# Kernel optimization log

Measured on AMD Instinct MI355X. Metric: run time of the kernel, lower is better.

The kernel has to match this reference:

```python
import jax, jax.numpy as jnp
import numpy as np

L, H, C, T_BLOCK, V = 12, 12, 768, 1024, 50257
EPS = 1e-5


def setup_inputs() -> dict:
    key = jax.random.key(0)
    ks = jax.random.split(key, 16)
    s = 0.02
    inp = {
        "idx": jax.random.randint(ks[0], (4, 1024), 0, V),
        "wte": jax.random.normal(ks[1], (V, C), jnp.float32) * s,
        "wpe": jax.random.normal(ks[2], (T_BLOCK, C), jnp.float32) * s,
        "ln1_w": jnp.ones((L, C), jnp.float32),
        "ln1_b": jnp.zeros((L, C), jnp.float32),
        "w_qkv": jax.random.normal(ks[3], (L, C, 3 * C), jnp.float32) * s,
        "b_qkv": jnp.zeros((L, 3 * C), jnp.float32),
        "w_ao": jax.random.normal(ks[4], (L, C, C), jnp.float32) * s,
        "b_ao": jnp.zeros((L, C), jnp.float32),
        "ln2_w": jnp.ones((L, C), jnp.float32),
        "ln2_b": jnp.zeros((L, C), jnp.float32),
        "w_fc": jax.random.normal(ks[5], (L, C, 4 * C), jnp.float32) * s,
        "b_fc": jnp.zeros((L, 4 * C), jnp.float32),
        "w_fp": jax.random.normal(ks[6], (L, 4 * C, C), jnp.float32) * s,
        "b_fp": jnp.zeros((L, C), jnp.float32),
        "lnf_w": jnp.ones((C,), jnp.float32),
        "lnf_b": jnp.zeros((C,), jnp.float32),
        "w_head": jax.random.normal(ks[7], (C, 1), jnp.float32) * s,
    }
    return inp


def _ln(x, w, b):
    mu = jnp.mean(x, axis=-1, keepdims=True)
    var = jnp.var(x, axis=-1, keepdims=True)
    return (x - mu) * jax.lax.rsqrt(var + EPS) * w + b


def _gpt_forward(idx, wte, wpe, ln1_w, ln1_b, w_qkv, b_qkv, w_ao, b_ao,
                 ln2_w, ln2_b, w_fc, b_fc, w_fp, b_fp, lnf_w, lnf_b, w_head):
    B, T = idx.shape
    D = C // H  # head dim
    x = wte[idx] + wpe[:T]  # [B,T,C]
    causal = jnp.tril(jnp.ones((T, T), bool))  # [T,T]

    def block(x, p):
        l1w, l1b, wq, bq, wo, bo, l2w, l2b, wf, bf, wp, bp = p
        h = _ln(x, l1w, l1b)
        qkv = h @ wq + bq  # [B,T,3C]
        q, k, v = jnp.split(qkv, 3, axis=-1)
        q = q.reshape(B, T, H, D).transpose(0, 2, 1, 3)  # [B,H,T,D]
        k = k.reshape(B, T, H, D).transpose(0, 2, 1, 3)
        v = v.reshape(B, T, H, D).transpose(0, 2, 1, 3)
        att = jnp.einsum('bhqd,bhkd->bhqk', q, k) * (1.0 / np.sqrt(D))
        att = jnp.where(causal, att, -jnp.inf)
        att = jax.nn.softmax(att, axis=-1)
        y = jnp.einsum('bhqk,bhkd->bhqd', att, v)
        y = y.transpose(0, 2, 1, 3).reshape(B, T, C)
        x = x + (y @ wo + bo)
        h2 = _ln(x, l2w, l2b)
        x = x + (jax.nn.gelu(h2 @ wf + bf, approximate=True) @ wp + bp)
        return x, None

    layer_params = (ln1_w, ln1_b, w_qkv, b_qkv, w_ao, b_ao,
                    ln2_w, ln2_b, w_fc, b_fc, w_fp, b_fp)
    x, _ = jax.lax.scan(block, x, layer_params)
    x = _ln(x, lnf_w, lnf_b)
    return x @ w_head  # [B,T,1]


def reference(idx, wte, wpe, ln1_w, ln1_b, w_qkv, b_qkv, w_ao, b_ao,
              ln2_w, ln2_b, w_fc, b_fc, w_fp, b_fp, lnf_w, lnf_b, w_head):
    return _gpt_forward(idx, wte, wpe, ln1_w, ln1_b, w_qkv, b_qkv, w_ao, b_ao,
                        ln2_w, ln2_b, w_fc, b_fc, w_fp, b_fp, lnf_w, lnf_b, w_head)
```

## Files before the change

kernel.cpp:

```cpp
#include <hip/hip_runtime.h>


#define CN    768
#define NKV   2304
#define FCN   3072
#define TN    1024
#define BN    4
#define HN    12
#define NL    12
#define MTOT  4096

typedef __attribute__((ext_vector_type(4))) float f32x4;
typedef __attribute__((ext_vector_type(8))) short short8;
typedef __attribute__((ext_vector_type(4))) unsigned short u16x4;

typedef const __attribute__((address_space(1))) void* gas_t;
typedef __attribute__((address_space(3))) void* las_t;

__device__ __forceinline__ unsigned short f2b(float f) {
    unsigned int u = __float_as_uint(f);
    u += 0x7fffu + ((u >> 16) & 1u);
    return (unsigned short)(u >> 16);
}
__device__ __forceinline__ float b2f(unsigned short h) {
    return __uint_as_float(((unsigned int)h) << 16);
}

__device__ __forceinline__ void gemm128(
        const unsigned short* __restrict__ A, int lda,
        const unsigned short* __restrict__ B, int ldb,
        int m0, int n0, int kbeg, int kend, f32x4 acc[4][4])
{
    __shared__ __align__(16) unsigned short As[128 * 32];
    __shared__ __align__(16) unsigned short Bs[128 * 32];
    const int tid  = threadIdx.x;
    const int wave = tid >> 6;
    const int lane = tid & 63;
    const int quad = lane >> 4;
    const int l16  = lane & 15;
    const int wm   = (wave & 1) * 64;
    const int wn   = (wave >> 1) * 64;
    const int srow = wave * 16 + (lane >> 2);
    const int scol = (lane & 3) << 3;
    const unsigned short* ag = A + (long)(m0 + srow) * lda + scol;
    const unsigned short* bg = B + (long)(n0 + srow) * ldb + scol;
    unsigned short* asw = As + wave * 512;
    unsigned short* bsw = Bs + wave * 512;

    for (int k0 = kbeg; k0 < kend; k0 += 32) {
        __syncthreads();
        __builtin_amdgcn_global_load_lds((gas_t)(ag + k0),                  (las_t)(asw),            16, 0, 0);
        __builtin_amdgcn_global_load_lds((gas_t)(ag + k0 + (long)64 * lda), (las_t)(asw + 64 * 32),  16, 0, 0);
        __builtin_amdgcn_global_load_lds((gas_t)(bg + k0),                  (las_t)(bsw),            16, 0, 0);
        __builtin_amdgcn_global_load_lds((gas_t)(bg + k0 + (long)64 * ldb), (las_t)(bsw + 64 * 32),  16, 0, 0);
        __syncthreads();
        short8 af[4], bf[4];
#pragma unroll
        for (int i = 0; i < 4; ++i)
            af[i] = *(const short8*)(As + (wm + i * 16 + l16) * 32 + quad * 8);
#pragma unroll
        for (int j = 0; j < 4; ++j)
            bf[j] = *(const short8*)(Bs + (wn + j * 16 + l16) * 32 + quad * 8);
#pragma unroll
        for (int i = 0; i < 4; ++i)
#pragma unroll
            for (int j = 0; j < 4; ++j)
                acc[i][j] = __builtin_amdgcn_mfma_f32_16x16x32_bf16(af[i], bf[j], acc[i][j], 0, 0, 0);
    }
}

__global__ __launch_bounds__(256) void k_qkv128(
        const unsigned short* __restrict__ A, const unsigned short* __restrict__ B,
        const float* __restrict__ bias,
        unsigned short* __restrict__ qb, unsigned short* __restrict__ kb,
        unsigned short* __restrict__ vt)
{
    f32x4 acc[4][4];
#pragma unroll
    for (int i = 0; i < 4; ++i)
#pragma unroll
        for (int j = 0; j < 4; ++j) acc[i][j] = 0.f;
    const int m0 = blockIdx.x * 128, n0 = blockIdx.y * 128;
    gemm128(A, CN, B, CN, m0, n0, 0, CN, acc);
    const int wave = threadIdx.x >> 6, lane = threadIdx.x & 63;
    const int quad = lane >> 4, l16 = lane & 15;
    const int wm = (wave & 1) * 64, wn = (wave >> 1) * 64;
#pragma unroll
    for (int j = 0; j < 4; ++j) {
        int col = n0 + wn + j * 16 + l16;
        float bv = bias[col];
        int which = col / CN;
        int cc = col - which * CN;
        int h = cc >> 6, d = cc & 63;
#pragma unroll
        for (int i = 0; i < 4; ++i) {
#pragma unroll
            for (int r = 0; r < 4; ++r) {
                int row = m0 + wm + i * 16 + quad * 4 + r;
                int b = row >> 10, t = row & 1023;
                int bh = b * HN + h;
                unsigned short val = f2b(acc[i][j][r] + bv);
                if (which == 0)      qb[(bh * TN + t) * 64 + d] = val;
                else if (which == 1) kb[(bh * TN + t) * 64 + d] = val;
                else                 vt[(bh * 64 + d) * TN + t] = val;
            }
        }
    }
}

__global__ __launch_bounds__(256) void k_fc128(
        const unsigned short* __restrict__ A, const unsigned short* __restrict__ B,
        const float* __restrict__ bias, unsigned short* __restrict__ G)
{
    f32x4 acc[4][4];
#pragma unroll
    for (int i = 0; i < 4; ++i)
#pragma unroll
        for (int j = 0; j < 4; ++j) acc[i][j] = 0.f;
    const int m0 = blockIdx.x * 128, n0 = blockIdx.y * 128;
    gemm128(A, CN, B, CN, m0, n0, 0, CN, acc);
    const int wave = threadIdx.x >> 6, lane = threadIdx.x & 63;
    const int quad = lane >> 4, l16 = lane & 15;
    const int wm = (wave & 1) * 64, wn = (wave >> 1) * 64;
#pragma unroll
    for (int j = 0; j < 4; ++j) {
        int col = n0 + wn + j * 16 + l16;
        float bv = bias[col];
#pragma unroll
        for (int i = 0; i < 4; ++i)
#pragma unroll
            for (int r = 0; r < 4; ++r) {
                int row = m0 + wm + i * 16 + quad * 4 + r;
                float u = acc[i][j][r] + bv;
                float c = 0.7978845608028654f * (u + 0.044715f * u * u * u);
                float g = 0.5f * u * (1.0f + tanhf(c));
                G[(long)row * FCN + col] = f2b(g);
            }
    }
}

__global__ __launch_bounds__(256) void k_res128(
        const unsigned short* __restrict__ A, int lda,
        const unsigned short* __restrict__ B, int K, int ksplit,
        const float* __restrict__ bias, float* __restrict__ X)
{
    f32x4 acc[4][4];
#pragma unroll
    for (int i = 0; i < 4; ++i)
#pragma unroll
        for (int j = 0; j < 4; ++j) acc[i][j] = 0.f;
    const int m0 = blockIdx.x * 128, n0 = blockIdx.y * 128;
    const int kz = blockIdx.z;
    const int klen = K / ksplit;
    gemm128(A, lda, B, K, m0, n0, kz * klen, kz * klen + klen, acc);
    const int wave = threadIdx.x >> 6, lane = threadIdx.x & 63;
    const int quad = lane >> 4, l16 = lane & 15;
    const int wm = (wave & 1) * 64, wn = (wave >> 1) * 64;
#pragma unroll
    for (int j = 0; j < 4; ++j) {
        int col = n0 + wn + j * 16 + l16;
        float bv = (kz == 0) ? bias[col] : 0.f;
#pragma unroll
        for (int i = 0; i < 4; ++i)
#pragma unroll
            for (int r = 0; r < 4; ++r) {
                int row = m0 + wm + i * 16 + quad * 4 + r;
                atomicAdd(&X[(long)row * CN + col], acc[i][j][r] + bv);
            }
    }
}

__device__ __forceinline__ void flash_qblock(
        int bm,
        const unsigned short* __restrict__ qg, const unsigned short* __restrict__ kg,
        const unsigned short* __restrict__ vg, unsigned short* __restrict__ yb,
        unsigned short* Qs, unsigned short* Ks, unsigned short* Vs,
        unsigned short* Ps)
{
    const int tid  = threadIdx.x;
    const int wave = tid >> 6;
    const int lane = tid & 63;
    const int quad = lane >> 4;
    const int l16  = lane & 15;
    const int r8 = lane >> 3;
    const int sl = lane & 7;

    __syncthreads();

#pragma unroll
    for (int c = 0; c < 4; ++c) {
        int chunk = wave * 4 + c;
        int row = chunk * 8 + r8;
        int slot = sl ^ (row & 7);
        __builtin_amdgcn_global_load_lds(
            (gas_t)(qg + (long)(bm * 128 + row) * 64 + slot * 8),
            (las_t)(Qs + chunk * 512), 16, 0, 0);
    }
    __syncthreads();

    short8 qf[2][2];
#pragma unroll
    for (int i = 0; i < 2; ++i)
#pragma unroll
        for (int ks = 0; ks < 2; ++ks) {
            int row = wave * 32 + i * 16 + l16;
            int slot = (ks * 4 + quad) ^ (row & 7);
            qf[i][ks] = *(const short8*)(Qs + row * 64 + slot * 8);
        }

    f32x4 acc[2][4];
#pragma unroll
    for (int i = 0; i < 2; ++i)
#pragma unroll
        for (int j = 0; j < 4; ++j) acc[i][j] = 0.f;
    float m_run[2][4], l_run[2][4];
#pragma unroll
    for (int i = 0; i < 2; ++i)
#pragma unroll
        for (int r = 0; r < 4; ++r) { m_run[i][r] = -3e38f; l_run[i][r] = 0.f; }

    const int qbase = bm * 128 + wave * 32;
    const int nt = 2 * bm + 2;
    unsigned short* pw = Ps + wave * (32 * 70);

    for (int t = 0; t < nt; ++t) {
        const int k0 = t * 64;
        __syncthreads();
#pragma unroll
        for (int c = 0; c < 2; ++c) {
            int chunk = wave * 2 + c;
            int row = chunk * 8 + r8;
            int slot = sl ^ (row & 7);
            __builtin_amdgcn_global_load_lds(
                (gas_t)(kg + (long)(k0 + row) * 64 + slot * 8),
                (las_t)(Ks + chunk * 512), 16, 0, 0);
            __builtin_amdgcn_global_load_lds(
                (gas_t)(vg + (long)row * TN + k0 + slot * 8),
                (las_t)(Vs + chunk * 512), 16, 0, 0);
        }
        __syncthreads();

        f32x4 s[2][4];
#pragma unroll
        for (int i = 0; i < 2; ++i)
#pragma unroll
            for (int j = 0; j < 4; ++j) s[i][j] = 0.f;
#pragma unroll
        for (int j = 0; j < 4; ++j) {
            int row = j * 16 + l16;
#pragma unroll
            for (int ks = 0; ks < 2; ++ks) {
                int slot = (ks * 4 + quad) ^ (row & 7);
                short8 kf = *(const short8*)(Ks + row * 64 + slot * 8);
#pragma unroll
                for (int i = 0; i < 2; ++i)
                    s[i][j] = __builtin_amdgcn_mfma_f32_16x16x32_bf16(qf[i][ks], kf, s[i][j], 0, 0, 0);
            }
        }

#pragma unroll
        for (int i = 0; i < 2; ++i) {
#pragma unroll
            for (int r = 0; r < 4; ++r) {
                const int qrow = qbase + i * 16 + quad * 4 + r;
                float mx = -3e38f;
#pragma unroll
                for (int j = 0; j < 4; ++j) {
                    float v = s[i][j][r] * 0.125f;
                    if (k0 + j * 16 + l16 > qrow) v = -3e38f;
                    s[i][j][r] = v;
                    mx = fmaxf(mx, v);
                }
#pragma unroll
                for (int o = 1; o < 16; o <<= 1) mx = fmaxf(mx, __shfl_xor(mx, o));
                const float mnew = fmaxf(m_run[i][r], mx);
                const float resc = __expf(m_run[i][r] - mnew);
                m_run[i][r] = mnew;
                float ls = 0.f;
#pragma unroll
                for (int j = 0; j < 4; ++j) {
                    float p = __expf(s[i][j][r] - mnew);
                    s[i][j][r] = p;
                    ls += p;
                }
#pragma unroll
                for (int o = 1; o < 16; o <<= 1) ls += __shfl_xor(ls, o);
                l_run[i][r] = l_run[i][r] * resc + ls;
#pragma unroll
                for (int j = 0; j < 4; ++j)
                    acc[i][j][r] *= resc;
            }
        }

#pragma unroll
        for (int i = 0; i < 2; ++i)
#pragma unroll
            for (int j = 0; j < 4; ++j)
#pragma unroll
                for (int r = 0; r < 4; ++r)
                    pw[(i * 16 + quad * 4 + r) * 70 + j * 16 + l16] = f2b(s[i][j][r]);
        __syncthreads();

        short8 pa[2][2];
#pragma unroll
        for (int i = 0; i < 2; ++i)
#pragma unroll
            for (int ks = 0; ks < 2; ++ks)
                pa[i][ks] = *(const short8*)(pw + (i * 16 + l16) * 70 + ks * 32 + quad * 8);

#pragma unroll
        for (int j = 0; j < 4; ++j) {
            int row = j * 16 + l16;
#pragma unroll
            for (int ks = 0; ks < 2; ++ks) {
                int slot = (ks * 4 + quad) ^ (row & 7);
                short8 vf = *(const short8*)(Vs + row * 64 + slot * 8);
#pragma unroll
                for (int i = 0; i < 2; ++i)
                    acc[i][j] = __builtin_amdgcn_mfma_f32_16x16x32_bf16(pa[i][ks], vf, acc[i][j], 0, 0, 0);
            }
        }
    }

#pragma unroll
    for (int i = 0; i < 2; ++i)
#pragma unroll
        for (int r = 0; r < 4; ++r) {
            const float inv = 1.0f / l_run[i][r];
            const int row = qbase + i * 16 + quad * 4 + r;
#pragma unroll
            for (int j = 0; j < 4; ++j)
                yb[(long)row * CN + j * 16 + l16] = f2b(acc[i][j][r] * inv);
        }
}

__global__ __launch_bounds__(256) void k_attn(
        const unsigned short* __restrict__ qb, const unsigned short* __restrict__ kb,
        const unsigned short* __restrict__ vt, unsigned short* __restrict__ y)
{
    __shared__ __align__(16) unsigned short Qs[128 * 64];
    __shared__ __align__(16) unsigned short Ks[64 * 64];
    __shared__ __align__(16) unsigned short Vs[64 * 64];
    __shared__ __align__(16) unsigned short Ps[4 * 32 * 70];

    const int x = blockIdx.x;
    const int z = blockIdx.z;
    const unsigned short* qg = qb + (long)z * TN * 64;
    const unsigned short* kg = kb + (long)z * TN * 64;
    const unsigned short* vg = vt + (long)z * 64 * TN;
    const int b = z / HN, h = z - b * HN;
    unsigned short* yb = y + (long)b * TN * CN + h * 64;

    flash_qblock(x,     qg, kg, vg, yb, Qs, Ks, Vs, Ps);
    flash_qblock(7 - x, qg, kg, vg, yb, Qs, Ks, Vs, Ps);
}

__global__ __launch_bounds__(256) void k_ln(
        const float* __restrict__ X, const float* __restrict__ w,
        const float* __restrict__ b, unsigned short* __restrict__ O)
{
    const int row  = blockIdx.x * 4 + (threadIdx.x >> 6);
    const int lane = threadIdx.x & 63;
    const f32x4* xr = (const f32x4*)(X + (long)row * CN);
    const f32x4* wv = (const f32x4*)w;
    const f32x4* bv = (const f32x4*)b;
    f32x4 v[3];
    float s = 0.f, sq = 0.f;
#pragma unroll
    for (int i = 0; i < 3; ++i) {
        v[i] = xr[i * 64 + lane];
#pragma unroll
        for (int c = 0; c < 4; ++c) { s += v[i][c]; sq += v[i][c] * v[i][c]; }
    }
#pragma unroll
    for (int o = 32; o > 0; o >>= 1) { s += __shfl_xor(s, o); sq += __shfl_xor(sq, o); }
    const float mu = s * (1.0f / CN);
    const float rstd = rsqrtf(sq * (1.0f / CN) - mu * mu + 1e-5f);
    u16x4* orow = (u16x4*)(O + (long)row * CN);
#pragma unroll
    for (int i = 0; i < 3; ++i) {
        f32x4 wc = wv[i * 64 + lane], bc = bv[i * 64 + lane];
        u16x4 o4;
#pragma unroll
        for (int c = 0; c < 4; ++c) o4[c] = f2b((v[i][c] - mu) * rstd * wc[c] + bc[c]);
        orow[i * 64 + lane] = o4;
    }
}

__global__ __launch_bounds__(256) void k_final(
        const float* __restrict__ X, const float* __restrict__ w,
        const float* __restrict__ b, const float* __restrict__ wh,
        float* __restrict__ out)
{
    const int row  = blockIdx.x * 4 + (threadIdx.x >> 6);
    const int lane = threadIdx.x & 63;
    const f32x4* xr = (const f32x4*)(X + (long)row * CN);
    const f32x4* wv = (const f32x4*)w;
    const f32x4* bv = (const f32x4*)b;
    const f32x4* hv = (const f32x4*)wh;
    f32x4 v[3];
    float s = 0.f, sq = 0.f;
#pragma unroll
    for (int i = 0; i < 3; ++i) {
        v[i] = xr[i * 64 + lane];
#pragma unroll
        for (int c = 0; c < 4; ++c) { s += v[i][c]; sq += v[i][c] * v[i][c]; }
    }
#pragma unroll
    for (int o = 32; o > 0; o >>= 1) { s += __shfl_xor(s, o); sq += __shfl_xor(sq, o); }
    const float mu = s * (1.0f / CN);
    const float rstd = rsqrtf(sq * (1.0f / CN) - mu * mu + 1e-5f);
    float acc = 0.f;
#pragma unroll
    for (int i = 0; i < 3; ++i) {
        f32x4 wc = wv[i * 64 + lane], bc = bv[i * 64 + lane], hc = hv[i * 64 + lane];
#pragma unroll
        for (int c = 0; c < 4; ++c)
            acc += ((v[i][c] - mu) * rstd * wc[c] + bc[c]) * hc[c];
    }
#pragma unroll
    for (int o = 32; o > 0; o >>= 1) acc += __shfl_xor(acc, o);
    if (lane == 0) out[row] = acc;
}

__global__ __launch_bounds__(256) void k_embed(
        const int* __restrict__ idx, const float* __restrict__ wte,
        const float* __restrict__ wpe, float* __restrict__ X)
{
    long i4 = (long)blockIdx.x * 256 + threadIdx.x;
    int c4 = (int)(i4 % (CN / 4));
    int bt = (int)(i4 / (CN / 4));
    int t = bt & 1023;
    int tok = idx[bt];
    f32x4 a = *(const f32x4*)(wte + (long)tok * CN + c4 * 4);
    f32x4 p = *(const f32x4*)(wpe + (long)t * CN + c4 * 4);
    *(f32x4*)(X + (long)bt * CN + c4 * 4) = a + p;
}

__global__ __launch_bounds__(256) void k_transpose(
        const float* __restrict__ in, unsigned short* __restrict__ out, int K, int N)
{
    __shared__ float tile[32][33];
    const int z = blockIdx.z;
    in  += (long)z * K * N;
    out += (long)z * K * N;
    const int n0 = blockIdx.x * 32, k0 = blockIdx.y * 32;
    const int tx = threadIdx.x & 31, ty = threadIdx.x >> 5;
#pragma unroll
    for (int i = 0; i < 4; ++i)
        tile[ty + i * 8][tx] = in[(long)(k0 + ty + i * 8) * N + n0 + tx];
    __syncthreads();
#pragma unroll
    for (int i = 0; i < 4; ++i)
        out[(long)(n0 + ty + i * 8) * K + k0 + tx] = f2b(tile[tx][ty + i * 8]);
}

extern "C" void kernel_launch(void* const* d_in, const int* in_sizes, int n_in,
                              void* d_out, int out_size, void* d_ws, size_t ws_size,
                              hipStream_t stream)
{
    const int*   idx    = (const int*)  d_in[0];
    const float* wte    = (const float*)d_in[1];
    const float* wpe    = (const float*)d_in[2];
    const float* ln1_w  = (const float*)d_in[3];
    const float* ln1_b  = (const float*)d_in[4];
    const float* w_qkv  = (const float*)d_in[5];
    const float* b_qkv  = (const float*)d_in[6];
    const float* w_ao   = (const float*)d_in[7];
    const float* b_ao   = (const float*)d_in[8];
    const float* ln2_w  = (const float*)d_in[9];
    const float* ln2_b  = (const float*)d_in[10];
    const float* w_fc   = (const float*)d_in[11];
    const float* b_fc   = (const float*)d_in[12];
    const float* w_fp   = (const float*)d_in[13];
    const float* b_fp   = (const float*)d_in[14];
    const float* lnf_w  = (const float*)d_in[15];
    const float* lnf_b  = (const float*)d_in[16];
    const float* w_head = (const float*)d_in[17];
    float* out = (float*)d_out;

    char* ws = (char*)d_ws;
    unsigned short* wqkvT = (unsigned short*)(ws + 0L);
    unsigned short* waoT  = (unsigned short*)(ws + 42467328L);
    unsigned short* wfcT  = (unsigned short*)(ws + 56623104L);
    unsigned short* wfpT  = (unsigned short*)(ws + 113246208L);
    float*          x     = (float*)         (ws + 169869312L);
    unsigned short* hb    = (unsigned short*)(ws + 182452224L);
    unsigned short* qb    = (unsigned short*)(ws + 188743680L);
    unsigned short* kb    = (unsigned short*)(ws + 195035136L);
    unsigned short* vt    = (unsigned short*)(ws + 201326592L);
    unsigned short* y     = (unsigned short*)(ws + 308281344L);
    unsigned short* g     = (unsigned short*)(ws + 314572800L);

    hipLaunchKernelGGL(k_transpose, dim3(NKV / 32, CN / 32, NL), dim3(256), 0, stream,
                       w_qkv, wqkvT, CN, NKV);
    hipLaunchKernelGGL(k_transpose, dim3(CN / 32, CN / 32, NL), dim3(256), 0, stream,
                       w_ao, waoT, CN, CN);
    hipLaunchKernelGGL(k_transpose, dim3(FCN / 32, CN / 32, NL), dim3(256), 0, stream,
                       w_fc, wfcT, CN, FCN);
    hipLaunchKernelGGL(k_transpose, dim3(CN / 32, FCN / 32, NL), dim3(256), 0, stream,
                       w_fp, wfpT, FCN, CN);

    hipLaunchKernelGGL(k_embed, dim3(MTOT * (CN / 4) / 256), dim3(256), 0, stream,
                       idx, wte, wpe, x);

    for (int l = 0; l < NL; ++l) {
        hipLaunchKernelGGL(k_ln, dim3(MTOT / 4), dim3(256), 0, stream,
                           x, ln1_w + l * CN, ln1_b + l * CN, hb);
        hipLaunchKernelGGL(k_qkv128, dim3(MTOT / 128, NKV / 128), dim3(256), 0, stream,
                           hb, wqkvT + (long)l * NKV * CN, b_qkv + l * NKV, qb, kb, vt);
        hipLaunchKernelGGL(k_attn, dim3(TN / 256, 1, BN * HN), dim3(256), 0, stream,
                           qb, kb, vt, y);
        hipLaunchKernelGGL(k_res128, dim3(MTOT / 128, CN / 128, 2), dim3(256), 0, stream,
                           y, CN, waoT + (long)l * CN * CN, CN, 2, b_ao + l * CN, x);
        hipLaunchKernelGGL(k_ln, dim3(MTOT / 4), dim3(256), 0, stream,
                           x, ln2_w + l * CN, ln2_b + l * CN, hb);
        hipLaunchKernelGGL(k_fc128, dim3(MTOT / 128, FCN / 128), dim3(256), 0, stream,
                           hb, wfcT + (long)l * FCN * CN, b_fc + l * FCN, g);
        hipLaunchKernelGGL(k_res128, dim3(MTOT / 128, CN / 128, 4), dim3(256), 0, stream,
                           g, FCN, wfpT + (long)l * FCN * CN, FCN, 4, b_fp + l * CN, x);
    }

    hipLaunchKernelGGL(k_final, dim3(MTOT / 4), dim3(256), 0, stream,
                       x, lnf_w, lnf_b, w_head, out);
}
```

Measured before the change: 3.239 ms.

## Replace split-K atomic residual adds with partial buffers reduced in fused LayerNorm

The split-K projection GEMMs now store their partial sums to separate fp32 buffers instead of doing atomicAdd into the residual stream. The following LayerNorm kernel (and the final LN/head kernel) sums the partials, adds the bias and the residual, writes x back, and normalizes. This removes scattered per-element atomics, which also made the summation order nondeterministic. The cost is extra fp32 partial traffic: each split writes and later reads a full 4096x768 tensor.

```diff
diff --git a/kernel.cpp b/kernel.cpp
--- a/kernel.cpp
+++ b/kernel.cpp
@@ -139,10 +139,10 @@
     }
 }
 
-__global__ __launch_bounds__(256) void k_res128(
+__global__ __launch_bounds__(256) void k_part128(
         const unsigned short* __restrict__ A, int lda,
         const unsigned short* __restrict__ B, int K, int ksplit,
-        const float* __restrict__ bias, float* __restrict__ X)
+        float* __restrict__ part)
 {
     f32x4 acc[4][4];
 #pragma unroll
@@ -153,19 +153,19 @@
     const int kz = blockIdx.z;
     const int klen = K / ksplit;
     gemm128(A, lda, B, K, m0, n0, kz * klen, kz * klen + klen, acc);
+    float* P = part + (long)kz * MTOT * CN;
     const int wave = threadIdx.x >> 6, lane = threadIdx.x & 63;
     const int quad = lane >> 4, l16 = lane & 15;
     const int wm = (wave & 1) * 64, wn = (wave >> 1) * 64;
 #pragma unroll
     for (int j = 0; j < 4; ++j) {
         int col = n0 + wn + j * 16 + l16;
-        float bv = (kz == 0) ? bias[col] : 0.f;
 #pragma unroll
         for (int i = 0; i < 4; ++i)
 #pragma unroll
             for (int r = 0; r < 4; ++r) {
                 int row = m0 + wm + i * 16 + quad * 4 + r;
-                atomicAdd(&X[(long)row * CN + col], acc[i][j][r] + bv);
+                P[(long)row * CN + col] = acc[i][j][r];
             }
     }
 }
@@ -355,23 +355,37 @@
     flash_qblock(7 - x, qg, kg, vg, yb, Qs, Ks, Vs, Ps);
 }
 
-__global__ __launch_bounds__(256) void k_ln(
-        const float* __restrict__ X, const float* __restrict__ w,
-        const float* __restrict__ b, unsigned short* __restrict__ O)
+__global__ __launch_bounds__(256) void k_lnr(
+        float* __restrict__ X, const float* __restrict__ part, int nparts,
+        const float* __restrict__ bias,
+        const float* __restrict__ w, const float* __restrict__ b,
+        unsigned short* __restrict__ O)
 {
     const int row  = blockIdx.x * 4 + (threadIdx.x >> 6);
     const int lane = threadIdx.x & 63;
-    const f32x4* xr = (const f32x4*)(X + (long)row * CN);
+    f32x4* xr = (f32x4*)(X + (long)row * CN);
     const f32x4* wv = (const f32x4*)w;
     const f32x4* bv = (const f32x4*)b;
     f32x4 v[3];
+#pragma unroll
+    for (int i = 0; i < 3; ++i) v[i] = xr[i * 64 + lane];
+    if (nparts > 0) {
+        const f32x4* bb = (const f32x4*)bias;
+#pragma unroll
+        for (int i = 0; i < 3; ++i) v[i] += bb[i * 64 + lane];
+        for (int p = 0; p < nparts; ++p) {
+            const f32x4* pr = (const f32x4*)(part + (long)p * MTOT * CN + (long)row * CN);
+#pragma unroll
+            for (int i = 0; i < 3; ++i) v[i] += pr[i * 64 + lane];
+        }
+#pragma unroll
+        for (int i = 0; i < 3; ++i) xr[i * 64 + lane] = v[i];
+    }
     float s = 0.f, sq = 0.f;
 #pragma unroll
-    for (int i = 0; i < 3; ++i) {
-        v[i] = xr[i * 64 + lane];
+    for (int i = 0; i < 3; ++i)
 #pragma unroll
         for (int c = 0; c < 4; ++c) { s += v[i][c]; sq += v[i][c] * v[i][c]; }
-    }
 #pragma unroll
     for (int o = 32; o > 0; o >>= 1) { s += __shfl_xor(s, o); sq += __shfl_xor(sq, o); }
     const float mu = s * (1.0f / CN);
@@ -387,10 +401,11 @@
     }
 }
 
-__global__ __launch_bounds__(256) void k_final(
-        const float* __restrict__ X, const float* __restrict__ w,
-        const float* __restrict__ b, const float* __restrict__ wh,
-        float* __restrict__ out)
+__global__ __launch_bounds__(256) void k_finalr(
+        const float* __restrict__ X, const float* __restrict__ part,
+        const float* __restrict__ bias,
+        const float* __restrict__ w, const float* __restrict__ b,
+        const float* __restrict__ wh, float* __restrict__ out)
 {
     const int row  = blockIdx.x * 4 + (threadIdx.x >> 6);
     const int lane = threadIdx.x & 63;
@@ -398,14 +413,20 @@
     const f32x4* wv = (const f32x4*)w;
     const f32x4* bv = (const f32x4*)b;
     const f32x4* hv = (const f32x4*)wh;
+    const f32x4* bb = (const f32x4*)bias;
     f32x4 v[3];
+#pragma unroll
+    for (int i = 0; i < 3; ++i) v[i] = xr[i * 64 + lane] + bb[i * 64 + lane];
+    for (int p = 0; p < 4; ++p) {
+        const f32x4* pr = (const f32x4*)(part + (long)p * MTOT * CN + (long)row * CN);
+#pragma unroll
+        for (int i = 0; i < 3; ++i) v[i] += pr[i * 64 + lane];
+    }
     float s = 0.f, sq = 0.f;
 #pragma unroll
-    for (int i = 0; i < 3; ++i) {
-        v[i] = xr[i * 64 + lane];
+    for (int i = 0; i < 3; ++i)
 #pragma unroll
         for (int c = 0; c < 4; ++c) { s += v[i][c]; sq += v[i][c] * v[i][c]; }
-    }
 #pragma unroll
     for (int o = 32; o > 0; o >>= 1) { s += __shfl_xor(s, o); sq += __shfl_xor(sq, o); }
     const float mu = s * (1.0f / CN);
@@ -489,6 +510,7 @@
     unsigned short* qb    = (unsigned short*)(ws + 188743680L);
     unsigned short* kb    = (unsigned short*)(ws + 195035136L);
     unsigned short* vt    = (unsigned short*)(ws + 201326592L);
+    float*          part  = (float*)         (ws + 207618048L);
     unsigned short* y     = (unsigned short*)(ws + 308281344L);
     unsigned short* g     = (unsigned short*)(ws + 314572800L);
 
@@ -505,22 +527,25 @@
                        idx, wte, wpe, x);
 
     for (int l = 0; l < NL; ++l) {
-        hipLaunchKernelGGL(k_ln, dim3(MTOT / 4), dim3(256), 0, stream,
-                           x, ln1_w + l * CN, ln1_b + l * CN, hb);
+        hipLaunchKernelGGL(k_lnr, dim3(MTOT / 4), dim3(256), 0, stream,
+                           x, part, (l == 0) ? 0 : 4,
+                           (l == 0) ? (const float*)nullptr : (b_fp + (l - 1) * CN),
+                           ln1_w + l * CN, ln1_b + l * CN, hb);
         hipLaunchKernelGGL(k_qkv128, dim3(MTOT / 128, NKV / 128), dim3(256), 0, stream,
                            hb, wqkvT + (long)l * NKV * CN, b_qkv + l * NKV, qb, kb, vt);
         hipLaunchKernelGGL(k_attn, dim3(TN / 256, 1, BN * HN), dim3(256), 0, stream,
                            qb, kb, vt, y);
-        hipLaunchKernelGGL(k_res128, dim3(MTOT / 128, CN / 128, 2), dim3(256), 0, stream,
-                           y, CN, waoT + (long)l * CN * CN, CN, 2, b_ao + l * CN, x);
-        hipLaunchKernelGGL(k_ln, dim3(MTOT / 4), dim3(256), 0, stream,
-                           x, ln2_w + l * CN, ln2_b + l * CN, hb);
+        hipLaunchKernelGGL(k_part128, dim3(MTOT / 128, CN / 128, 2), dim3(256), 0, stream,
+                           y, CN, waoT + (long)l * CN * CN, CN, 2, part);
+        hipLaunchKernelGGL(k_lnr, dim3(MTOT / 4), dim3(256), 0, stream,
+                           x, part, 2, b_ao + l * CN,
+                           ln2_w + l * CN, ln2_b + l * CN, hb);
         hipLaunchKernelGGL(k_fc128, dim3(MTOT / 128, FCN / 128), dim3(256), 0, stream,
                            hb, wfcT + (long)l * FCN * CN, b_fc + l * FCN, g);
-        hipLaunchKernelGGL(k_res128, dim3(MTOT / 128, CN / 128, 4), dim3(256), 0, stream,
-                           g, FCN, wfpT + (long)l * FCN * CN, FCN, 4, b_fp + l * CN, x);
-    }
-
-    hipLaunchKernelGGL(k_final, dim3(MTOT / 4), dim3(256), 0, stream,
-                       x, lnf_w, lnf_b, w_head, out);
-}
+        hipLaunchKernelGGL(k_part128, dim3(MTOT / 128, CN / 128, 4), dim3(256), 0, stream,
+                           g, FCN, wfpT + (long)l * FCN * CN, FCN, 4, part);
+    }
+
+    hipLaunchKernelGGL(k_finalr, dim3(MTOT / 4), dim3(256), 0, stream,
+                       x, part, b_fp + (NL - 1) * CN, lnf_w, lnf_b, w_head, out);
+}
```

Result: faster. 2.945 ms (-9.1%).
